# Performance work log

Hardware: AMD Instinct MI355X
Metric: run time of the kernel (lower is better)

The kernel has to match this reference:

```python
import jax, jax.numpy as jnp
import numpy as np

B, N, C, H = 4, 1024, 768, 12
D = C // H  # head_dim = 64
EPS_BN = 1e-5


def setup_inputs() -> dict:
    key = jax.random.key(0)
    ks = jax.random.split(key, 8)
    s = np.float32(D ** -0.5)
    return {
        "x": jax.random.normal(ks[0], (B, N, C), dtype=jnp.float32),
        "qkv_w": jax.random.normal(ks[1], (3 * C, C), dtype=jnp.float32) * (C ** -0.5),
        "qkv_b": jnp.zeros((3 * C,), dtype=jnp.float32),
        "proj_w": jax.random.normal(ks[2], (C, C), dtype=jnp.float32) * (C ** -0.5),
        "proj_b": jnp.zeros((C,), dtype=jnp.float32),
        "scale": jnp.asarray(s),
        "riem_scale": jnp.asarray(s),
        "grass_scale": jnp.asarray(s),
        "conv_w": jax.random.normal(ks[3], (H, 3 * H), dtype=jnp.float32) * ((3 * H) ** -0.5),
        "conv_b": jnp.zeros((H,), dtype=jnp.float32),
        "bn_gamma": jnp.ones((H,), dtype=jnp.float32),
        "bn_beta": jnp.zeros((H,), dtype=jnp.float32),
        "bn_mean": jnp.zeros((H,), dtype=jnp.float32),
        "bn_var": jnp.ones((H,), dtype=jnp.float32),
    }


def reference(x, qkv_w, qkv_b, proj_w, proj_b, scale, riem_scale, grass_scale,
              conv_w, conv_b, bn_gamma, bn_beta, bn_mean, bn_var):
    Bx, Nx, Cx = x.shape
    # qkv projection -> [3, B, H, N, D]
    qkv = (x @ qkv_w.T + qkv_b).reshape(Bx, Nx, 3, H, D).transpose(2, 0, 3, 1, 4)
    q, k, v = qkv[0], qkv[1], qkv[2]

    # Grassmannian points: reduced QR over each [N, D] token matrix
    qgr, _ = jnp.linalg.qr(q)
    kgr, _ = jnp.linalg.qr(k)
    # dots [B,H,N,N]; norm over singleton dim == abs, then squared -> dots**2
    dots = jnp.einsum('bhnd,bhmd->bhnm', qgr, kgr)
    attn_grass = (dots * dots) * grass_scale

    # standard scaled dot-product scores
    qk = jnp.einsum('bhnd,bhmd->bhnm', q, k)
    attn = qk * scale

    # covariance Frobenius distance between rank-1 covariances q_i q_i^T, k_j k_j^T:
    # ||q q^T - k k^T||_F^2 = |q|^4 + |k|^4 - 2 (q.k)^2 ; similarity = -sqrt(.)
    qn2 = jnp.sum(q * q, axis=-1)  # [B,H,N]
    kn2 = jnp.sum(k * k, axis=-1)  # [B,H,N]
    d2 = qn2[..., :, None] ** 2 + kn2[..., None, :] ** 2 - 2.0 * (qk * qk)
    attn_riem = -jnp.sqrt(jnp.maximum(d2, 0.0) + 1e-8) * riem_scale

    # concat over head-channel dim -> [B, 3H, N, N], 1x1 conv + BatchNorm (eval stats)
    cat = jnp.concatenate([attn, attn_riem, attn_grass], axis=1)
    y = jnp.einsum('bcnm,oc->bonm', cat, conv_w) + conv_b[None, :, None, None]
    inv = (bn_gamma / jnp.sqrt(bn_var + EPS_BN))[None, :, None, None]
    y = (y - bn_mean[None, :, None, None]) * inv + bn_beta[None, :, None, None]

    p = jax.nn.softmax(y, axis=-1)
    out = jnp.einsum('bhnm,bhmd->bhnd', p, v)  # [B,H,N,D]
    out = out.transpose(0, 2, 1, 3).reshape(Bx, Nx, Cx)
    return out @ proj_w.T + proj_b
```

## Files before the change

kernel.cpp:

```cpp
#include <hip/hip_runtime.h>
#include <math.h>


typedef __attribute__((ext_vector_type(8))) short short8;
typedef __attribute__((ext_vector_type(4))) float f32x4;

__device__ __forceinline__ unsigned bf16r(float x) {
    unsigned u = __float_as_uint(x);
    return (u + 0x7FFFu + ((u >> 16) & 1u)) >> 16;
}
__device__ __forceinline__ unsigned packhl(float x) {
    unsigned u = __float_as_uint(x);
    unsigned hi = (u + 0x7FFFu + ((u >> 16) & 1u)) & 0xFFFF0000u;
    float lo = x - __uint_as_float(hi);
    unsigned ul = __float_as_uint(lo);
    unsigned l16 = (ul + 0x7FFFu + ((ul >> 16) & 1u)) >> 16;
    return hi | (l16 & 0xFFFFu);
}
__device__ __forceinline__ uint4 pack4(float4 v) {
    uint4 o;
    o.x = packhl(v.x); o.y = packhl(v.y); o.z = packhl(v.z); o.w = packhl(v.w);
    return o;
}
__device__ __forceinline__ float unpackhl(unsigned u) {
    return __uint_as_float(u & 0xFFFF0000u) + __uint_as_float(u << 16);
}
union U4S8 { uint4 u; short8 s; };
__device__ __forceinline__ short8 mk_hi(uint4 a, uint4 b) {
    U4S8 r;
    r.u.x = __builtin_amdgcn_perm(a.y, a.x, 0x07060302);
    r.u.y = __builtin_amdgcn_perm(a.w, a.z, 0x07060302);
    r.u.z = __builtin_amdgcn_perm(b.y, b.x, 0x07060302);
    r.u.w = __builtin_amdgcn_perm(b.w, b.z, 0x07060302);
    return r.s;
}
__device__ __forceinline__ short8 mk_lo(uint4 a, uint4 b) {
    U4S8 r;
    r.u.x = __builtin_amdgcn_perm(a.y, a.x, 0x05040100);
    r.u.y = __builtin_amdgcn_perm(a.w, a.z, 0x05040100);
    r.u.z = __builtin_amdgcn_perm(b.y, b.x, 0x05040100);
    r.u.w = __builtin_amdgcn_perm(b.w, b.z, 0x05040100);
    return r.s;
}
__device__ __forceinline__ uint4 ld4v(const unsigned* vp, int mbase, int d) {
    uint4 r;
    r.x = vp[(size_t)(mbase + 0) * 64 + d];
    r.y = vp[(size_t)(mbase + 1) * 64 + d];
    r.z = vp[(size_t)(mbase + 2) * 64 + d];
    r.w = vp[(size_t)(mbase + 3) * 64 + d];
    return r;
}
#define MFMA(a,b,c) __builtin_amdgcn_mfma_f32_16x16x32_bf16(a, b, c, 0, 0, 0)

__global__ __launch_bounds__(256) void qkv_mfma(
    const float* __restrict__ x, const float* __restrict__ wsrc,
    const float* __restrict__ bias,
    float* __restrict__ q, float* __restrict__ k,
    unsigned* __restrict__ qpk, unsigned* __restrict__ kpk, unsigned* __restrict__ vpk)
{
    __shared__ unsigned xT[32 * 64];
    __shared__ unsigned wT[64 * 64];
    const int tid = threadIdx.x;
    const int lane = tid & 63;
    const int w = tid >> 6;
    const int rowL = lane & 15;
    const int g = lane >> 4;
    const int r7 = rowL & 7;
    const int n0 = blockIdx.x * 64;
    const int m0 = blockIdx.y * 32;
    f32x4 accA = {0,0,0,0}, accB = {0,0,0,0};

    for (int kk0 = 0; kk0 < 768; kk0 += 64) {
        __syncthreads();
#pragma unroll
        for (int e = 0; e < 2; e++) {
            int ci = tid + 256 * e; int R = ci >> 4, c = ci & 15;
            float4 fv = *(const float4*)&x[(size_t)(m0 + R) * 768 + kk0 + c * 4];
            *(uint4*)&xT[R * 64 + ((c ^ (R & 7)) << 2)] = pack4(fv);
        }
#pragma unroll
        for (int e = 0; e < 4; e++) {
            int ci = tid + 256 * e; int R = ci >> 4, c = ci & 15;
            float4 fv = *(const float4*)&wsrc[(size_t)(n0 + R) * 768 + kk0 + c * 4];
            *(uint4*)&wT[R * 64 + ((c ^ (R & 7)) << 2)] = pack4(fv);
        }
        __syncthreads();
#pragma unroll
        for (int ks = 0; ks < 2; ks++) {
            int c0 = ks * 8 + g * 2;
            uint4 b0 = *(const uint4*)&wT[(w * 16 + rowL) * 64 + ((c0 ^ r7) << 2)];
            uint4 b1 = *(const uint4*)&wT[(w * 16 + rowL) * 64 + (((c0 + 1) ^ r7) << 2)];
            short8 whi = mk_hi(b0, b1), wlo = mk_lo(b0, b1);
            uint4 a0 = *(const uint4*)&xT[rowL * 64 + ((c0 ^ r7) << 2)];
            uint4 a1 = *(const uint4*)&xT[rowL * 64 + (((c0 + 1) ^ r7) << 2)];
            short8 xhi = mk_hi(a0, a1), xlo = mk_lo(a0, a1);
            accA = MFMA(xhi, whi, accA);
            accA = MFMA(xhi, wlo, accA);
            accA = MFMA(xlo, whi, accA);
            uint4 a2 = *(const uint4*)&xT[(16 + rowL) * 64 + ((c0 ^ r7) << 2)];
            uint4 a3 = *(const uint4*)&xT[(16 + rowL) * 64 + (((c0 + 1) ^ r7) << 2)];
            short8 xhi2 = mk_hi(a2, a3), xlo2 = mk_lo(a2, a3);
            accB = MFMA(xhi2, whi, accB);
            accB = MFMA(xhi2, wlo, accB);
            accB = MFMA(xlo2, whi, accB);
        }
    }
    const int col = n0 + w * 16 + rowL;
    const float bv = bias[col];
    const int s = (n0 >= 1536) ? 2 : ((n0 >= 768) ? 1 : 0);
    const int hc = col - s * 768;
    const int head = hc >> 6;
    const int cin = hc & 63;
#pragma unroll
    for (int half = 0; half < 2; half++) {
        f32x4 acc = half ? accB : accA;
#pragma unroll
        for (int r = 0; r < 4; r++) {
            int row = m0 + half * 16 + g * 4 + r;
            int bb = row >> 10, n = row & 1023;
            size_t idx = ((size_t)(bb * 12 + head) << 16) + ((size_t)n << 6) + cin;
            float val = acc[r] + bv;
            if (s == 0)      { q[idx] = val; qpk[idx] = packhl(val); }
            else if (s == 1) { k[idx] = val; kpk[idx] = packhl(val); }
            else             { vpk[idx] = packhl(val); }
        }
    }
}

__global__ __launch_bounds__(256) void proj_mfma(
    const unsigned* __restrict__ apk, const float* __restrict__ wsrc,
    const float* __restrict__ bias, float* __restrict__ out)
{
    __shared__ unsigned xT[32 * 64];
    __shared__ unsigned wT[64 * 64];
    const int tid = threadIdx.x;
    const int lane = tid & 63;
    const int w = tid >> 6;
    const int rowL = lane & 15;
    const int g = lane >> 4;
    const int r7 = rowL & 7;
    const int n0 = blockIdx.x * 64;
    const int m0 = blockIdx.y * 32;
    f32x4 accA = {0,0,0,0}, accB = {0,0,0,0};

    for (int kk0 = 0; kk0 < 768; kk0 += 64) {
        __syncthreads();
#pragma unroll
        for (int e = 0; e < 2; e++) {
            int ci = tid + 256 * e; int R = ci >> 4, c = ci & 15;
            uint4 v = *(const uint4*)&apk[(size_t)(m0 + R) * 768 + kk0 + c * 4];
            *(uint4*)&xT[R * 64 + ((c ^ (R & 7)) << 2)] = v;
        }
#pragma unroll
        for (int e = 0; e < 4; e++) {
            int ci = tid + 256 * e; int R = ci >> 4, c = ci & 15;
            float4 fv = *(const float4*)&wsrc[(size_t)(n0 + R) * 768 + kk0 + c * 4];
            *(uint4*)&wT[R * 64 + ((c ^ (R & 7)) << 2)] = pack4(fv);
        }
        __syncthreads();
#pragma unroll
        for (int ks = 0; ks < 2; ks++) {
            int c0 = ks * 8 + g * 2;
            uint4 b0 = *(const uint4*)&wT[(w * 16 + rowL) * 64 + ((c0 ^ r7) << 2)];
            uint4 b1 = *(const uint4*)&wT[(w * 16 + rowL) * 64 + (((c0 + 1) ^ r7) << 2)];
            short8 whi = mk_hi(b0, b1), wlo = mk_lo(b0, b1);
            uint4 a0 = *(const uint4*)&xT[rowL * 64 + ((c0 ^ r7) << 2)];
            uint4 a1 = *(const uint4*)&xT[rowL * 64 + (((c0 + 1) ^ r7) << 2)];
            short8 xhi = mk_hi(a0, a1), xlo = mk_lo(a0, a1);
            accA = MFMA(xhi, whi, accA);
            accA = MFMA(xhi, wlo, accA);
            accA = MFMA(xlo, whi, accA);
            uint4 a2 = *(const uint4*)&xT[(16 + rowL) * 64 + ((c0 ^ r7) << 2)];
            uint4 a3 = *(const uint4*)&xT[(16 + rowL) * 64 + (((c0 + 1) ^ r7) << 2)];
            short8 xhi2 = mk_hi(a2, a3), xlo2 = mk_lo(a2, a3);
            accB = MFMA(xhi2, whi, accB);
            accB = MFMA(xhi2, wlo, accB);
            accB = MFMA(xlo2, whi, accB);
        }
    }
    const int col = n0 + w * 16 + rowL;
    const float bv = bias[col];
#pragma unroll
    for (int half = 0; half < 2; half++) {
        f32x4 acc = half ? accB : accA;
#pragma unroll
        for (int r = 0; r < 4; r++) {
            int row = m0 + half * 16 + g * 4 + r;
            out[(size_t)row * 768 + col] = acc[r] + bv;
        }
    }
}

__global__ __launch_bounds__(256) void row_norms(
    const float* __restrict__ q, const float* __restrict__ k,
    float* __restrict__ qn4, float* __restrict__ kn4)
{
    int wid = blockIdx.x * 4 + (threadIdx.x >> 6);
    int lane = threadIdx.x & 63;
    const float* src; float* dst; int r;
    if (wid < 49152) { src = q; dst = qn4; r = wid; }
    else             { src = k; dst = kn4; r = wid - 49152; }
    float xv = src[(size_t)r * 64 + lane];
    float s = xv * xv;
#pragma unroll
    for (int m = 1; m < 64; m <<= 1) s += __shfl_xor(s, m, 64);
    if (lane == 0) dst[r] = s * s;
}

__global__ __launch_bounds__(1024)
__attribute__((amdgpu_waves_per_eu(4, 4)))
void qr_fact(const float* __restrict__ q, const float* __restrict__ k,
             unsigned* __restrict__ Vp_, float* __restrict__ taug)
{
    const int id = blockIdx.x;
    const float* src = (id & 1) ? k : q;
    src += (size_t)(id >> 1) << 16;
    unsigned* Vp = Vp_ + (size_t)id * 65536;
    const int tid = threadIdx.x;
    const int lane = tid & 63;
    const int w = tid >> 6;
    __shared__ float vbufA[1024];
    __shared__ float vbufB[1024];
    __shared__ float taub[64];

    float a[4][16];
#pragma unroll
    for (int c = 0; c < 4; c++)
#pragma unroll
        for (int i = 0; i < 16; i++)
            a[c][i] = src[(i * 64 + lane) * 64 + 4 * w + c];

    if (w == 0) {
        float part = 0.f;
#pragma unroll
        for (int i = 0; i < 16; i++) part += a[0][i] * a[0][i];
#pragma unroll
        for (int m = 1; m < 64; m <<= 1) part += __shfl_xor(part, m, 64);
        float sigma = part;
        float xd = __shfl(a[0][0], 0, 64);
        float nrm = sqrtf(sigma);
        float beta = (xd >= 0.f) ? -nrm : nrm;
        float vd = xd - beta;
        float vtv = (sigma - xd * xd) + vd * vd;
        float tau2 = (vtv > 0.f) ? 2.f / vtv : 0.f;
        if (lane == 0) a[0][0] = vd;
#pragma unroll
        for (int i = 0; i < 16; i++) vbufA[i * 64 + lane] = a[0][i];
        if (lane == 0) taub[0] = tau2;
    }
    __syncthreads();

    for (int d = 0; d < 64; d++) {
        const int jb = 4 * w;
        if (jb + 3 > d) {
            float* vb = (d & 1) ? vbufB : vbufA;
            float vr[16];
#pragma unroll
            for (int i = 0; i < 16; i++) vr[i] = vb[i * 64 + lane];
            float t2 = taub[d];
            float dp0 = 0.f, dp1 = 0.f, dp2 = 0.f, dp3 = 0.f;
#pragma unroll
            for (int i = 0; i < 16; i++) {
                dp0 += vr[i] * a[0][i];
                dp1 += vr[i] * a[1][i];
                dp2 += vr[i] * a[2][i];
                dp3 += vr[i] * a[3][i];
            }
#pragma unroll
            for (int m = 1; m < 64; m <<= 1) {
                dp0 += __shfl_xor(dp0, m, 64);
                dp1 += __shfl_xor(dp1, m, 64);
                dp2 += __shfl_xor(dp2, m, 64);
                dp3 += __shfl_xor(dp3, m, 64);
            }
            float s0 = t2 * dp0, s1 = t2 * dp1, s2 = t2 * dp2, s3 = t2 * dp3;
            if (jb + 0 > d) {
#pragma unroll
                for (int i = 0; i < 16; i++) a[0][i] -= s0 * vr[i];
            }
            if (jb + 1 > d) {
#pragma unroll
                for (int i = 0; i < 16; i++) a[1][i] -= s1 * vr[i];
            }
            if (jb + 2 > d) {
#pragma unroll
                for (int i = 0; i < 16; i++) a[2][i] -= s2 * vr[i];
            }
            {
#pragma unroll
                for (int i = 0; i < 16; i++) a[3][i] -= s3 * vr[i];
            }
        }
        if (d < 63) {
            const int dn = d + 1;
            if (w == (dn >> 2)) {
                const int cd = dn & 3;
#pragma unroll
                for (int c = 0; c < 4; c++) if (c == cd) {
                    float part = 0.f;
#pragma unroll
                    for (int i = 0; i < 16; i++) {
                        int r = i * 64 + lane;
                        float xx = a[c][i];
                        part += (r >= dn) ? xx * xx : 0.f;
                    }
#pragma unroll
                    for (int m = 1; m < 64; m <<= 1) part += __shfl_xor(part, m, 64);
                    float sigma = part;
                    float xd = __shfl(a[c][0], dn, 64);
                    float nrm = sqrtf(sigma);
                    float beta = (xd >= 0.f) ? -nrm : nrm;
                    float vd = xd - beta;
                    float vtv = (sigma - xd * xd) + vd * vd;
                    float tau2 = (vtv > 0.f) ? 2.f / vtv : 0.f;
                    if (lane == dn) a[c][0] = vd;
                    float* vbn = (dn & 1) ? vbufB : vbufA;
#pragma unroll
                    for (int i = 0; i < 16; i++) {
                        int r = i * 64 + lane;
                        vbn[i * 64 + lane] = (r < dn) ? 0.f : a[c][i];
                    }
                    if (lane == 0) taub[dn] = tau2;
                }
            }
        }
        __syncthreads();
    }

    if (tid < 64) taug[id * 64 + tid] = taub[tid];
#pragma unroll
    for (int c = 0; c < 4; c++) {
        int j = 4 * w + c;
#pragma unroll
        for (int i = 0; i < 16; i++) {
            int r = i * 64 + lane;
            float vv = (r < j) ? 0.f : a[c][i];
            Vp[(size_t)j * 1024 + r] = packhl(vv);
        }
    }
}

__global__ __launch_bounds__(256) void qr_gpart(
    const unsigned* __restrict__ Vp_, float* __restrict__ Gpart)
{
    const int id = blockIdx.x;
    const int sl = blockIdx.y;
    const unsigned* Vp = Vp_ + (size_t)id * 65536;
    __shared__ unsigned Vc[64 * 32];
    const int tid = threadIdx.x;
    const int lane = tid & 63;
    const int w = tid >> 6;
    const int rowL = lane & 15;
    const int g = lane >> 4;

    f32x4 acc0 = {0,0,0,0}, acc1 = {0,0,0,0}, acc2 = {0,0,0,0}, acc3 = {0,0,0,0};
    for (int r0 = sl * 256; r0 < sl * 256 + 256; r0 += 32) {
        __syncthreads();
#pragma unroll
        for (int e = 0; e < 2; e++) {
            int ci = tid + 256 * e;
            int row = ci >> 3, c = ci & 7;
            uint4 v = *(const uint4*)&Vp[(size_t)row * 1024 + r0 + c * 4];
            *(uint4*)&Vc[row * 32 + ((c ^ (row & 7)) << 2)] = v;
        }
        __syncthreads();
        int ra = w * 16 + rowL;
        uint4 a0 = *(const uint4*)&Vc[ra * 32 + (((g * 2) ^ (ra & 7)) << 2)];
        uint4 a1 = *(const uint4*)&Vc[ra * 32 + (((g * 2 + 1) ^ (ra & 7)) << 2)];
        short8 Ahi = mk_hi(a0, a1), Alo = mk_lo(a0, a1);
#define GDO(jt, accv) { int rb = jt * 16 + rowL; \
        uint4 b0 = *(const uint4*)&Vc[rb * 32 + (((g * 2) ^ (rb & 7)) << 2)]; \
        uint4 b1 = *(const uint4*)&Vc[rb * 32 + (((g * 2 + 1) ^ (rb & 7)) << 2)]; \
        short8 Bhi = mk_hi(b0, b1), Blo = mk_lo(b0, b1); \
        accv = MFMA(Ahi, Bhi, accv); accv = MFMA(Ahi, Blo, accv); accv = MFMA(Alo, Bhi, accv); }
        GDO(0, acc0) GDO(1, acc1) GDO(2, acc2) GDO(3, acc3)
#undef GDO
    }
    float* dst = Gpart + ((size_t)(id * 4 + sl) << 12);
#define GWR(jt, accv) { \
    dst[(w * 16 + g * 4 + 0) * 64 + jt * 16 + rowL] = accv[0]; \
    dst[(w * 16 + g * 4 + 1) * 64 + jt * 16 + rowL] = accv[1]; \
    dst[(w * 16 + g * 4 + 2) * 64 + jt * 16 + rowL] = accv[2]; \
    dst[(w * 16 + g * 4 + 3) * 64 + jt * 16 + rowL] = accv[3]; }
    GWR(0, acc0) GWR(1, acc1) GWR(2, acc2) GWR(3, acc3)
#undef GWR
}

__global__ __launch_bounds__(256) void qr_tw2(
    const unsigned* __restrict__ Vp_, const float* __restrict__ taug,
    const float* __restrict__ Gpart, float* __restrict__ Wg)
{
    const int id = blockIdx.x;
    const unsigned* Vp = Vp_ + (size_t)id * 65536;
    __shared__ float G_s[64 * 65];
    __shared__ float wbuf[64];
    __shared__ float tau_s[64];
    const int tid = threadIdx.x;
    if (tid < 64) tau_s[tid] = taug[id * 64 + tid];
    const float* Gp = Gpart + ((size_t)(id * 4) << 12);
#pragma unroll
    for (int e = 0; e < 16; e++) {
        int idx = tid + 256 * e;
        float sum = Gp[idx] + Gp[4096 + idx] + Gp[8192 + idx] + Gp[12288 + idx];
        G_s[(idx >> 6) * 65 + (idx & 63)] = sum;
    }
    const int i = tid >> 2;
    const int cq = tid & 3;
    float regA[16];
#pragma unroll
    for (int cc = 0; cc < 16; cc++)
        regA[cc] = unpackhl(Vp[(size_t)i * 1024 + cq * 16 + cc]);
    __syncthreads();
    for (int j = 63; j >= 0; j--) {
        if (i == j) {
            float tj = tau_s[j];
#pragma unroll
            for (int cc = 0; cc < 16; cc++) {
                regA[cc] *= tj;
                wbuf[cq * 16 + cc] = regA[cc];
            }
        }
        __syncthreads();
        if (i < j) {
            float gij = G_s[i * 65 + j];
#pragma unroll
            for (int cc = 0; cc < 16; cc++)
                regA[cc] = fmaf(-gij, wbuf[cq * 16 + cc], regA[cc]);
        }
        __syncthreads();
    }
#pragma unroll
    for (int cc = 0; cc < 16; cc++)
        Wg[(size_t)id * 4096 + i * 64 + cq * 16 + cc] = regA[cc];
}

__global__ __launch_bounds__(256) void qr_formq(
    const unsigned* __restrict__ Vp_, const float* __restrict__ Wg,
    unsigned short* __restrict__ qgrh, unsigned short* __restrict__ kgrh)
{
    const int id = blockIdx.x;
    const int rb = blockIdx.y;
    const unsigned* Vp = Vp_ + (size_t)id * 65536;
    const float* Wm = Wg + (size_t)id * 4096;
    unsigned short* dst = ((id & 1) ? kgrh : qgrh) + ((size_t)(id >> 1) << 16);
    __shared__ float Vl[64 * 65];
    __shared__ float Wl[64 * 64];
    const int tid = threadIdx.x;
    const int rbase = rb * 64;
#pragma unroll
    for (int e = 0; e < 16; e++) {
        int idx = tid + 256 * e;
        int j = idx >> 6, rl = idx & 63;
        Vl[rl * 65 + j] = unpackhl(Vp[(size_t)j * 1024 + rbase + rl]);
        Wl[idx] = Wm[idx];
    }
    __syncthreads();
    const int rl = tid >> 2;
    const int cg = (tid & 3) << 4;
    const int rglob = rbase + rl;
    unsigned short outv[16];
#pragma unroll
    for (int cc = 0; cc < 16; cc++) {
        int c = cg + cc;
        float s = (rglob == c) ? 1.f : 0.f;
        for (int j = 0; j < 64; j++) s -= Vl[rl * 65 + j] * Wl[j * 64 + c];
        outv[cc] = (unsigned short)bf16r(s);
    }
#pragma unroll
    for (int cc = 0; cc < 16; cc += 4)
        *(ushort4*)&dst[(size_t)rglob * 64 + cg + cc] = *(ushort4*)&outv[cc];
}

#define SC_EACH12(F) F(0) F(1) F(2) F(3) F(4) F(5) F(6) F(7) F(8) F(9) F(10) F(11)
#define SC_DECLY(o) float y##o##_0 = 0.f, y##o##_1 = 0.f, y##o##_2 = 0.f, y##o##_3 = 0.f;
#define SC_LOADC(o) const float cA##o = cw[o * 36 + h], \
                                cB##o = cw[o * 36 + 12 + h], \
                                cC##o = cw[o * 36 + 24 + h];
#define SC_CONV1(o,r) y##o##_##r = fmaf(cA##o, att, fmaf(cB##o, rie, fmaf(cC##o, gra, y##o##_##r)));
#define SC_CONVROW(r) SC_CONV1(0,r) SC_CONV1(1,r) SC_CONV1(2,r) SC_CONV1(3,r) SC_CONV1(4,r) SC_CONV1(5,r) \
                      SC_CONV1(6,r) SC_CONV1(7,r) SC_CONV1(8,r) SC_CONV1(9,r) SC_CONV1(10,r) SC_CONV1(11,r)
#define SC_SCORE(r) { \
    float qk = s1[r], gr = s2[r]; \
    float qn4v = qn4s[g * 4 + r]; \
    float att = qk * scale; \
    float d2 = qn4v + kn4v - 2.f * qk * qk; \
    float rie = -sqrtf(fmaxf(d2, 0.f) + 1e-8f) * riem_scale; \
    float gra = gr * gr * grass_scale; \
    SC_CONVROW(r) }
#define SC_OUT(o) { \
    float inv = bn_gamma[o] * rsqrtf(bn_var[o] + 1e-5f); \
    float Bb = fmaf(conv_b[o] - bn_mean[o], inv, bn_beta[o]); \
    float* dst = Sbuf + ((size_t)(z * 12 + o) * 1024 + n0) * 1024 + m0 + w * 16 + rowL; \
    dst[(size_t)(g * 4 + 0) * 1024] = fmaf(y##o##_0, inv, Bb); \
    dst[(size_t)(g * 4 + 1) * 1024] = fmaf(y##o##_1, inv, Bb); \
    dst[(size_t)(g * 4 + 2) * 1024] = fmaf(y##o##_2, inv, Bb); \
    dst[(size_t)(g * 4 + 3) * 1024] = fmaf(y##o##_3, inv, Bb); }

__global__ __launch_bounds__(256) void sattn_scores(
    const unsigned* __restrict__ qpk, const unsigned* __restrict__ kpk,
    const unsigned short* __restrict__ qgrh, const unsigned short* __restrict__ kgrh,
    const float* __restrict__ qn4g, const float* __restrict__ kn4g,
    const float* __restrict__ cw, const float* __restrict__ conv_b,
    const float* __restrict__ bn_gamma, const float* __restrict__ bn_beta,
    const float* __restrict__ bn_mean, const float* __restrict__ bn_var,
    const float* __restrict__ scale_p, const float* __restrict__ riem_p,
    const float* __restrict__ grass_p, float* __restrict__ Sbuf, int b0)
{
    __shared__ unsigned qT[16 * 64];
    __shared__ unsigned short qgT[16 * 64];
    __shared__ unsigned kL[64 * 64];
    __shared__ unsigned short kgrL[64 * 64];
    __shared__ float qn4s[16];
    __shared__ float kn4s[64];

    const int tid = threadIdx.x;
    const int lane = tid & 63;
    const int w = tid >> 6;
    const int rowL = lane & 15;
    const int g = lane >> 4;
    const int r7 = rowL & 7;
    const int m0 = blockIdx.x * 64;
    const int n0 = blockIdx.y * 16;
    const int z = blockIdx.z;
    const int b = b0 + z;
    const float scale = scale_p[0], riem_scale = riem_p[0], grass_scale = grass_p[0];

    SC_EACH12(SC_DECLY)

    for (int h = 0; h < 12; h++) {
        __syncthreads();
        {
            int R = tid >> 4, c = tid & 15;
            uint4 v = *(const uint4*)&qpk[((size_t)(b * 12 + h) << 16) + (size_t)(n0 + R) * 64 + c * 4];
            *(uint4*)&qT[R * 64 + ((c ^ (R & 7)) << 2)] = v;
        }
        if (tid < 128) {
            int R = tid >> 3, c = tid & 7;
            uint4 v = *(const uint4*)&qgrh[((size_t)(b * 12 + h) << 16) + (size_t)(n0 + R) * 64 + c * 8];
            *(uint4*)&qgT[R * 64 + ((c ^ (R & 7)) << 3)] = v;
        }
#pragma unroll
        for (int e = 0; e < 4; e++) {
            int ci = tid + 256 * e; int m = ci >> 4, c = ci & 15;
            uint4 v = *(const uint4*)&kpk[((size_t)(b * 12 + h) << 16) + (size_t)(m0 + m) * 64 + c * 4];
            *(uint4*)&kL[m * 64 + ((c ^ (m & 7)) << 2)] = v;
        }
#pragma unroll
        for (int e = 0; e < 2; e++) {
            int ci = tid + 256 * e; int m = ci >> 3, c = ci & 7;
            uint4 v = *(const uint4*)&kgrh[((size_t)(b * 12 + h) << 16) + (size_t)(m0 + m) * 64 + c * 8];
            *(uint4*)&kgrL[m * 64 + ((c ^ (m & 7)) << 3)] = v;
        }
        if (tid < 64) kn4s[tid] = kn4g[(size_t)(b * 12 + h) * 1024 + m0 + tid];
        if (tid < 16) qn4s[tid] = qn4g[(size_t)(b * 12 + h) * 1024 + n0 + tid];
        __syncthreads();

        float kn4v = kn4s[w * 16 + rowL];
        f32x4 s1 = {0,0,0,0}, s2 = {0,0,0,0};
#pragma unroll
        for (int ks = 0; ks < 2; ks++) {
            int c0 = ks * 8 + g * 2;
            uint4 a0 = *(const uint4*)&qT[rowL * 64 + ((c0 ^ r7) << 2)];
            uint4 a1 = *(const uint4*)&qT[rowL * 64 + (((c0 + 1) ^ r7) << 2)];
            uint4 b0v = *(const uint4*)&kL[(w * 16 + rowL) * 64 + ((c0 ^ r7) << 2)];
            uint4 b1v = *(const uint4*)&kL[(w * 16 + rowL) * 64 + (((c0 + 1) ^ r7) << 2)];
            short8 qhi = mk_hi(a0, a1), qlo = mk_lo(a0, a1);
            short8 khi = mk_hi(b0v, b1v), klo = mk_lo(b0v, b1v);
            s1 = MFMA(qhi, khi, s1);
            s1 = MFMA(qhi, klo, s1);
            s1 = MFMA(qlo, khi, s1);
            int cg = ks * 4 + g;
            short8 qg = *(const short8*)&qgT[rowL * 64 + ((cg ^ r7) << 3)];
            short8 kg2 = *(const short8*)&kgrL[(w * 16 + rowL) * 64 + ((cg ^ r7) << 3)];
            s2 = MFMA(qg, kg2, s2);
        }
        SC_EACH12(SC_LOADC)
        SC_SCORE(0) SC_SCORE(1) SC_SCORE(2) SC_SCORE(3)
    }
    SC_EACH12(SC_OUT)
}

__global__ __launch_bounds__(256) void sattn_pv(
    const unsigned* __restrict__ vpk, const float* __restrict__ Sbuf,
    unsigned* __restrict__ attno_pk, int b0)
{
    __shared__ unsigned short P_s[16 * 64];
    __shared__ unsigned vt_s[64 * 64];
    __shared__ float mrun[16], lrun[16], cos_[16];

    const int tid = threadIdx.x;
    const int lane = tid & 63;
    const int w = tid >> 6;
    const int rowL = lane & 15;
    const int g = lane >> 4;
    const int r7 = rowL & 7;
    const int n0 = blockIdx.x * 16;
    const int o = blockIdx.y;
    const int z = blockIdx.z;
    const int b = b0 + z;
    const int srow = tid >> 4;
    const int sc4 = (tid & 15) * 4;

    if (tid < 16) { mrun[tid] = -1e30f; lrun[tid] = 0.f; }
    f32x4 acc = {0,0,0,0};
    const float* Srow = Sbuf + ((size_t)(z * 12 + o) * 1024 + n0 + srow) * 1024;
    const unsigned* vp = vpk + ((size_t)(b * 12 + o) << 16);
    __syncthreads();

    for (int m0 = 0; m0 < 1024; m0 += 64) {
        float4 sv = *(const float4*)&Srow[m0 + sc4];
        float mx = fmaxf(fmaxf(sv.x, sv.y), fmaxf(sv.z, sv.w));
        mx = fmaxf(mx, __shfl_xor(mx, 1, 64));
        mx = fmaxf(mx, __shfl_xor(mx, 2, 64));
        mx = fmaxf(mx, __shfl_xor(mx, 4, 64));
        mx = fmaxf(mx, __shfl_xor(mx, 8, 64));
        float mo = mrun[srow];
        float mn = fmaxf(mo, mx);
        float co = expf(mo - mn);
        float p0 = expf(sv.x - mn), p1 = expf(sv.y - mn), p2 = expf(sv.z - mn), p3 = expf(sv.w - mn);
        unsigned u0 = bf16r(p0), u1 = bf16r(p1), u2 = bf16r(p2), u3 = bf16r(p3);
        {
            ushort4 pw = make_ushort4((unsigned short)u0, (unsigned short)u1,
                                      (unsigned short)u2, (unsigned short)u3);
            *(ushort4*)&P_s[srow * 64 + (((sc4 >> 3) ^ (srow & 7)) << 3) + (sc4 & 7)] = pw;
        }
        float ps = __uint_as_float(u0 << 16) + __uint_as_float(u1 << 16)
                 + __uint_as_float(u2 << 16) + __uint_as_float(u3 << 16);
        ps += __shfl_xor(ps, 1, 64); ps += __shfl_xor(ps, 2, 64);
        ps += __shfl_xor(ps, 4, 64); ps += __shfl_xor(ps, 8, 64);
        if ((lane & 15) == 0) {
            mrun[srow] = mn;
            cos_[srow] = co;
            lrun[srow] = lrun[srow] * co + ps;
        }
#pragma unroll
        for (int e = 0; e < 4; e++) {
            int d_ = tid & 63;
            int mb = (tid >> 6) * 4 + 16 * e;
            int mc = (tid >> 6) + 4 * e;
            uint4 v = ld4v(vp + (size_t)m0 * 64, mb, d_);
            *(uint4*)&vt_s[d_ * 64 + ((mc ^ (d_ & 15)) << 2)] = v;
        }
        __syncthreads();
        {
            float c0_ = cos_[g * 4 + 0], c1_ = cos_[g * 4 + 1];
            float c2_ = cos_[g * 4 + 2], c3_ = cos_[g * 4 + 3];
            acc[0] *= c0_; acc[1] *= c1_; acc[2] *= c2_; acc[3] *= c3_;
        }
        const int d_ = w * 16 + rowL;
        const unsigned* vrow = &vt_s[d_ * 64];
#pragma unroll
        for (int kk = 0; kk < 2; kk++) {
            int mc8 = kk * 4 + g;
            short8 pa = *(const short8*)&P_s[rowL * 64 + ((mc8 ^ r7) << 3)];
            int c0 = kk * 8 + g * 2;
            uint4 b0v = *(const uint4*)&vrow[((c0 ^ (d_ & 15)) << 2)];
            uint4 b1v = *(const uint4*)&vrow[(((c0 + 1) ^ (d_ & 15)) << 2)];
            short8 vh = mk_hi(b0v, b1v), vl = mk_lo(b0v, b1v);
            acc = MFMA(pa, vh, acc);
            acc = MFMA(pa, vl, acc);
        }
        __syncthreads();
    }
#pragma unroll
    for (int r = 0; r < 4; r++) {
        int row = g * 4 + r;
        size_t idx = ((size_t)(b * 1024 + n0 + row)) * 768 + o * 64 + w * 16 + rowL;
        attno_pk[idx] = packhl(acc[r] / lrun[row]);
    }
}

extern "C" void kernel_launch(void* const* d_in, const int* in_sizes, int n_in,
                              void* d_out, int out_size, void* d_ws, size_t ws_size,
                              hipStream_t stream) {
    const float* x          = (const float*)d_in[0];
    const float* qkv_w      = (const float*)d_in[1];
    const float* qkv_b      = (const float*)d_in[2];
    const float* proj_w     = (const float*)d_in[3];
    const float* proj_b     = (const float*)d_in[4];
    const float* scale      = (const float*)d_in[5];
    const float* riem_scale = (const float*)d_in[6];
    const float* grass_scale= (const float*)d_in[7];
    const float* conv_w     = (const float*)d_in[8];
    const float* conv_b     = (const float*)d_in[9];
    const float* bn_gamma   = (const float*)d_in[10];
    const float* bn_beta    = (const float*)d_in[11];
    const float* bn_mean    = (const float*)d_in[12];
    const float* bn_var     = (const float*)d_in[13];
    float* out = (float*)d_out;

    float* q   = (float*)d_ws;
    float* k   = q + 3145728;
    unsigned* qpk = (unsigned*)(k + 3145728);
    unsigned* kpk = qpk + 3145728;
    unsigned* vpk = kpk + 3145728;
    unsigned short* qgrh = (unsigned short*)(vpk + 3145728);
    unsigned short* kgrh = qgrh + 3145728;
    float* qn4 = (float*)(kgrh + 3145728);
    float* kn4 = qn4 + 49152;
    unsigned* attno_pk = (unsigned*)q;

    const size_t BASE = 75890688ull;
    const size_t SB1  = 50331648ull;
    float* Sbuf = (float*)((char*)d_ws + BASE);
    unsigned* Vpk2 = (unsigned*)((char*)d_ws + BASE);
    float* Wg   = (float*)(Vpk2 + 96 * 65536);
    float* taug = Wg + 96 * 4096;
    float* Gpart = taug + 96 * 64;
    const bool full = (ws_size >= BASE + 4 * SB1);

    hipLaunchKernelGGL(qkv_mfma, dim3(36, 128), dim3(256), 0, stream,
                       x, qkv_w, qkv_b, q, k, qpk, kpk, vpk);
    hipLaunchKernelGGL(row_norms, dim3(24576), dim3(256), 0, stream, q, k, qn4, kn4);

    hipLaunchKernelGGL(qr_fact, dim3(96), dim3(1024), 0, stream, q, k, Vpk2, taug);
    hipLaunchKernelGGL(qr_gpart, dim3(96, 4), dim3(256), 0, stream, Vpk2, Gpart);
    hipLaunchKernelGGL(qr_tw2, dim3(96), dim3(256), 0, stream, Vpk2, taug, Gpart, Wg);
    hipLaunchKernelGGL(qr_formq, dim3(96, 16), dim3(256), 0, stream, Vpk2, Wg, qgrh, kgrh);

    if (full) {
        hipLaunchKernelGGL(sattn_scores, dim3(16, 64, 4), dim3(256), 0, stream,
                           qpk, kpk, qgrh, kgrh, qn4, kn4, conv_w, conv_b,
                           bn_gamma, bn_beta, bn_mean, bn_var,
                           scale, riem_scale, grass_scale, Sbuf, 0);
        hipLaunchKernelGGL(sattn_pv, dim3(64, 12, 4), dim3(256), 0, stream,
                           vpk, Sbuf, attno_pk, 0);
    } else {
        for (int b = 0; b < 4; b++) {
            hipLaunchKernelGGL(sattn_scores, dim3(16, 64, 1), dim3(256), 0, stream,
                               qpk, kpk, qgrh, kgrh, qn4, kn4, conv_w, conv_b,
                               bn_gamma, bn_beta, bn_mean, bn_var,
                               scale, riem_scale, grass_scale, Sbuf, b);
            hipLaunchKernelGGL(sattn_pv, dim3(64, 12, 1), dim3(256), 0, stream,
                               vpk, Sbuf, attno_pk, b);
        }
    }

    hipLaunchKernelGGL(proj_mfma, dim3(12, 128), dim3(256), 0, stream,
                       attno_pk, proj_w, proj_b, out);
}
```

Before: 683.2 us.

## Pre-pack GEMM operands to hi/lo bf16 once and enlarge qkv tile

Adds a pack_f32 kernel that converts x, qkv_w and proj_w into packed hi/lo bf16 words once, so the qkv and projection GEMMs load pre-packed tiles instead of repeating the split per block. The qkv GEMM tile grows from 32 to 64 rows, with four accumulators per wave, to reuse each weight tile across more rows. This adds extra kernel launches and a round trip through workspace memory, and raises register and LDS use in the qkv kernel.

```diff
diff --git a/kernel.cpp b/kernel.cpp
--- a/kernel.cpp
+++ b/kernel.cpp
@@ -16,11 +16,6 @@
     unsigned ul = __float_as_uint(lo);
     unsigned l16 = (ul + 0x7FFFu + ((ul >> 16) & 1u)) >> 16;
     return hi | (l16 & 0xFFFFu);
-}
-__device__ __forceinline__ uint4 pack4(float4 v) {
-    uint4 o;
-    o.x = packhl(v.x); o.y = packhl(v.y); o.z = packhl(v.z); o.w = packhl(v.w);
-    return o;
 }
 __device__ __forceinline__ float unpackhl(unsigned u) {
     return __uint_as_float(u & 0xFFFF0000u) + __uint_as_float(u << 16);
@@ -52,11 +47,92 @@
 }
 #define MFMA(a,b,c) __builtin_amdgcn_mfma_f32_16x16x32_bf16(a, b, c, 0, 0, 0)
 
+__global__ __launch_bounds__(256) void pack_f32(
+    const float* __restrict__ src, unsigned* __restrict__ dst, int n4)
+{
+    int i = blockIdx.x * 256 + threadIdx.x;
+    if (i < n4) {
+        float4 v = *(const float4*)&src[(size_t)i * 4];
+        uint4 o;
+        o.x = packhl(v.x); o.y = packhl(v.y); o.z = packhl(v.z); o.w = packhl(v.w);
+        *(uint4*)&dst[(size_t)i * 4] = o;
+    }
+}
+
 __global__ __launch_bounds__(256) void qkv_mfma(
-    const float* __restrict__ x, const float* __restrict__ wsrc,
+    const unsigned* __restrict__ xpk, const unsigned* __restrict__ wpk,
     const float* __restrict__ bias,
     float* __restrict__ q, float* __restrict__ k,
     unsigned* __restrict__ qpk, unsigned* __restrict__ kpk, unsigned* __restrict__ vpk)
+{
+    __shared__ unsigned xT[64 * 64];
+    __shared__ unsigned wT[64 * 64];
+    const int tid = threadIdx.x;
+    const int lane = tid & 63;
+    const int w = tid >> 6;
+    const int rowL = lane & 15;
+    const int g = lane >> 4;
+    const int r7 = rowL & 7;
+    const int n0 = blockIdx.x * 64;
+    const int m0 = blockIdx.y * 64;
+    f32x4 acc0 = {0,0,0,0}, acc1 = {0,0,0,0}, acc2 = {0,0,0,0}, acc3 = {0,0,0,0};
+
+    for (int kk0 = 0; kk0 < 768; kk0 += 64) {
+        __syncthreads();
+#pragma unroll
+        for (int e = 0; e < 4; e++) {
+            int ci = tid + 256 * e; int R = ci >> 4, c = ci & 15;
+            uint4 v = *(const uint4*)&xpk[(size_t)(m0 + R) * 768 + kk0 + c * 4];
+            *(uint4*)&xT[R * 64 + ((c ^ (R & 7)) << 2)] = v;
+        }
+#pragma unroll
+        for (int e = 0; e < 4; e++) {
+            int ci = tid + 256 * e; int R = ci >> 4, c = ci & 15;
+            uint4 v = *(const uint4*)&wpk[(size_t)(n0 + R) * 768 + kk0 + c * 4];
+            *(uint4*)&wT[R * 64 + ((c ^ (R & 7)) << 2)] = v;
+        }
+        __syncthreads();
+#pragma unroll
+        for (int ks = 0; ks < 2; ks++) {
+            int c0 = ks * 8 + g * 2;
+            uint4 b0 = *(const uint4*)&wT[(w * 16 + rowL) * 64 + ((c0 ^ r7) << 2)];
+            uint4 b1 = *(const uint4*)&wT[(w * 16 + rowL) * 64 + (((c0 + 1) ^ r7) << 2)];
+            short8 whi = mk_hi(b0, b1), wlo = mk_lo(b0, b1);
+#define QFRAG(f, accv) { \
+            uint4 a0 = *(const uint4*)&xT[(f * 16 + rowL) * 64 + ((c0 ^ r7) << 2)]; \
+            uint4 a1 = *(const uint4*)&xT[(f * 16 + rowL) * 64 + (((c0 + 1) ^ r7) << 2)]; \
+            short8 xhi = mk_hi(a0, a1), xlo = mk_lo(a0, a1); \
+            accv = MFMA(xhi, whi, accv); \
+            accv = MFMA(xhi, wlo, accv); \
+            accv = MFMA(xlo, whi, accv); }
+            QFRAG(0, acc0) QFRAG(1, acc1) QFRAG(2, acc2) QFRAG(3, acc3)
+#undef QFRAG
+        }
+    }
+    const int col = n0 + w * 16 + rowL;
+    const float bv = bias[col];
+    const int s = (n0 >= 1536) ? 2 : ((n0 >= 768) ? 1 : 0);
+    const int hc = col - s * 768;
+    const int head = hc >> 6;
+    const int cin = hc & 63;
+#define QOUT(f, accv) { \
+    _Pragma("unroll") \
+    for (int r = 0; r < 4; r++) { \
+        int row = m0 + f * 16 + g * 4 + r; \
+        int bb = row >> 10, n = row & 1023; \
+        size_t idx = ((size_t)(bb * 12 + head) << 16) + ((size_t)n << 6) + cin; \
+        float val = accv[r] + bv; \
+        if (s == 0)      { q[idx] = val; qpk[idx] = packhl(val); } \
+        else if (s == 1) { k[idx] = val; kpk[idx] = packhl(val); } \
+        else             { vpk[idx] = packhl(val); } \
+    } }
+    QOUT(0, acc0) QOUT(1, acc1) QOUT(2, acc2) QOUT(3, acc3)
+#undef QOUT
+}
+
+__global__ __launch_bounds__(256) void proj_mfma(
+    const unsigned* __restrict__ apk, const unsigned* __restrict__ wpk,
+    const float* __restrict__ bias, float* __restrict__ out)
 {
     __shared__ unsigned xT[32 * 64];
     __shared__ unsigned wT[64 * 64];
@@ -75,87 +151,14 @@
 #pragma unroll
         for (int e = 0; e < 2; e++) {
             int ci = tid + 256 * e; int R = ci >> 4, c = ci & 15;
-            float4 fv = *(const float4*)&x[(size_t)(m0 + R) * 768 + kk0 + c * 4];
-            *(uint4*)&xT[R * 64 + ((c ^ (R & 7)) << 2)] = pack4(fv);
+            uint4 v = *(const uint4*)&apk[(size_t)(m0 + R) * 768 + kk0 + c * 4];
+            *(uint4*)&xT[R * 64 + ((c ^ (R & 7)) << 2)] = v;
         }
 #pragma unroll
         for (int e = 0; e < 4; e++) {
             int ci = tid + 256 * e; int R = ci >> 4, c = ci & 15;
-            float4 fv = *(const float4*)&wsrc[(size_t)(n0 + R) * 768 + kk0 + c * 4];
-            *(uint4*)&wT[R * 64 + ((c ^ (R & 7)) << 2)] = pack4(fv);
-        }
-        __syncthreads();
-#pragma unroll
-        for (int ks = 0; ks < 2; ks++) {
-            int c0 = ks * 8 + g * 2;
-            uint4 b0 = *(const uint4*)&wT[(w * 16 + rowL) * 64 + ((c0 ^ r7) << 2)];
-            uint4 b1 = *(const uint4*)&wT[(w * 16 + rowL) * 64 + (((c0 + 1) ^ r7) << 2)];
-            short8 whi = mk_hi(b0, b1), wlo = mk_lo(b0, b1);
-            uint4 a0 = *(const uint4*)&xT[rowL * 64 + ((c0 ^ r7) << 2)];
-            uint4 a1 = *(const uint4*)&xT[rowL * 64 + (((c0 + 1) ^ r7) << 2)];
-            short8 xhi = mk_hi(a0, a1), xlo = mk_lo(a0, a1);
-            accA = MFMA(xhi, whi, accA);
-            accA = MFMA(xhi, wlo, accA);
-            accA = MFMA(xlo, whi, accA);
-            uint4 a2 = *(const uint4*)&xT[(16 + rowL) * 64 + ((c0 ^ r7) << 2)];
-            uint4 a3 = *(const uint4*)&xT[(16 + rowL) * 64 + (((c0 + 1) ^ r7) << 2)];
-            short8 xhi2 = mk_hi(a2, a3), xlo2 = mk_lo(a2, a3);
-            accB = MFMA(xhi2, whi, accB);
-            accB = MFMA(xhi2, wlo, accB);
-            accB = MFMA(xlo2, whi, accB);
-        }
-    }
-    const int col = n0 + w * 16 + rowL;
-    const float bv = bias[col];
-    const int s = (n0 >= 1536) ? 2 : ((n0 >= 768) ? 1 : 0);
-    const int hc = col - s * 768;
-    const int head = hc >> 6;
-    const int cin = hc & 63;
-#pragma unroll
-    for (int half = 0; half < 2; half++) {
-        f32x4 acc = half ? accB : accA;
-#pragma unroll
-        for (int r = 0; r < 4; r++) {
-            int row = m0 + half * 16 + g * 4 + r;
-            int bb = row >> 10, n = row & 1023;
-            size_t idx = ((size_t)(bb * 12 + head) << 16) + ((size_t)n << 6) + cin;
-            float val = acc[r] + bv;
-            if (s == 0)      { q[idx] = val; qpk[idx] = packhl(val); }
-            else if (s == 1) { k[idx] = val; kpk[idx] = packhl(val); }
-            else             { vpk[idx] = packhl(val); }
-        }
-    }
-}
-
-__global__ __launch_bounds__(256) void proj_mfma(
-    const unsigned* __restrict__ apk, const float* __restrict__ wsrc,
-    const float* __restrict__ bias, float* __restrict__ out)
-{
-    __shared__ unsigned xT[32 * 64];
-    __shared__ unsigned wT[64 * 64];
-    const int tid = threadIdx.x;
-    const int lane = tid & 63;
-    const int w = tid >> 6;
-    const int rowL = lane & 15;
-    const int g = lane >> 4;
-    const int r7 = rowL & 7;
-    const int n0 = blockIdx.x * 64;
-    const int m0 = blockIdx.y * 32;
-    f32x4 accA = {0,0,0,0}, accB = {0,0,0,0};
-
-    for (int kk0 = 0; kk0 < 768; kk0 += 64) {
-        __syncthreads();
-#pragma unroll
-        for (int e = 0; e < 2; e++) {
-            int ci = tid + 256 * e; int R = ci >> 4, c = ci & 15;
-            uint4 v = *(const uint4*)&apk[(size_t)(m0 + R) * 768 + kk0 + c * 4];
-            *(uint4*)&xT[R * 64 + ((c ^ (R & 7)) << 2)] = v;
-        }
-#pragma unroll
-        for (int e = 0; e < 4; e++) {
-            int ci = tid + 256 * e; int R = ci >> 4, c = ci & 15;
-            float4 fv = *(const float4*)&wsrc[(size_t)(n0 + R) * 768 + kk0 + c * 4];
-            *(uint4*)&wT[R * 64 + ((c ^ (R & 7)) << 2)] = pack4(fv);
+            uint4 v = *(const uint4*)&wpk[(size_t)(n0 + R) * 768 + kk0 + c * 4];
+            *(uint4*)&wT[R * 64 + ((c ^ (R & 7)) << 2)] = v;
         }
         __syncthreads();
 #pragma unroll
@@ -699,24 +702,31 @@
     float* qn4 = (float*)(kgrh + 3145728);
     float* kn4 = qn4 + 49152;
     unsigned* attno_pk = (unsigned*)q;
+    unsigned* ppk = (unsigned*)k;
 
     const size_t BASE = 75890688ull;
     const size_t SB1  = 50331648ull;
     float* Sbuf = (float*)((char*)d_ws + BASE);
+    unsigned* xpk_ = (unsigned*)((char*)d_ws + BASE);
+    unsigned* wpk_ = xpk_ + 3145728;
     unsigned* Vpk2 = (unsigned*)((char*)d_ws + BASE);
     float* Wg   = (float*)(Vpk2 + 96 * 65536);
     float* taug = Wg + 96 * 4096;
     float* Gpart = taug + 96 * 64;
     const bool full = (ws_size >= BASE + 4 * SB1);
 
-    hipLaunchKernelGGL(qkv_mfma, dim3(36, 128), dim3(256), 0, stream,
-                       x, qkv_w, qkv_b, q, k, qpk, kpk, vpk);
+    hipLaunchKernelGGL(pack_f32, dim3(3072), dim3(256), 0, stream, x, xpk_, 786432);
+    hipLaunchKernelGGL(pack_f32, dim3(1728), dim3(256), 0, stream, qkv_w, wpk_, 442368);
+    hipLaunchKernelGGL(qkv_mfma, dim3(36, 64), dim3(256), 0, stream,
+                       xpk_, wpk_, qkv_b, q, k, qpk, kpk, vpk);
     hipLaunchKernelGGL(row_norms, dim3(24576), dim3(256), 0, stream, q, k, qn4, kn4);
 
     hipLaunchKernelGGL(qr_fact, dim3(96), dim3(1024), 0, stream, q, k, Vpk2, taug);
     hipLaunchKernelGGL(qr_gpart, dim3(96, 4), dim3(256), 0, stream, Vpk2, Gpart);
     hipLaunchKernelGGL(qr_tw2, dim3(96), dim3(256), 0, stream, Vpk2, taug, Gpart, Wg);
     hipLaunchKernelGGL(qr_formq, dim3(96, 16), dim3(256), 0, stream, Vpk2, Wg, qgrh, kgrh);
+
+    hipLaunchKernelGGL(pack_f32, dim3(576), dim3(256), 0, stream, proj_w, ppk, 147456);
 
     if (full) {
         hipLaunchKernelGGL(sattn_scores, dim3(16, 64, 4), dim3(256), 0, stream,
@@ -737,5 +747,5 @@
     }
 
     hipLaunchKernelGGL(proj_mfma, dim3(12, 128), dim3(256), 0, stream,
-                       attno_pk, proj_w, proj_b, out);
-}
+                       attno_pk, ppk, proj_b, out);
+}
```

Result: no change. 693.4 us (+1.5%).

## Pre-pack GEMM operands to bf16 pairs and enlarge score tile to 32 rows

Applied to the files above, without the earlier changes.

Adds a pack_f32 kernel that converts x, qkv_w and proj_w once into hi/lo bf16 packed words, so the qkv and proj GEMMs no longer repeat the split conversion in every tile load. The sattn_scores kernel now uses 512 threads and 32 query rows per block, so each loaded K tile is reused across twice as many rows and the grid is halved. The trade-off is three extra launches plus the memory traffic of the packed copies, and higher shared memory and register pressure per block in the scores kernel. The packed buffers reuse workspace regions (the Sbuf area and the k buffer) and rely on those regions not being live at the time.

```diff
diff --git a/kernel.cpp b/kernel.cpp
--- a/kernel.cpp
+++ b/kernel.cpp
@@ -16,11 +16,6 @@
     unsigned ul = __float_as_uint(lo);
     unsigned l16 = (ul + 0x7FFFu + ((ul >> 16) & 1u)) >> 16;
     return hi | (l16 & 0xFFFFu);
-}
-__device__ __forceinline__ uint4 pack4(float4 v) {
-    uint4 o;
-    o.x = packhl(v.x); o.y = packhl(v.y); o.z = packhl(v.z); o.w = packhl(v.w);
-    return o;
 }
 __device__ __forceinline__ float unpackhl(unsigned u) {
     return __uint_as_float(u & 0xFFFF0000u) + __uint_as_float(u << 16);
@@ -52,8 +47,20 @@
 }
 #define MFMA(a,b,c) __builtin_amdgcn_mfma_f32_16x16x32_bf16(a, b, c, 0, 0, 0)
 
+__global__ __launch_bounds__(256) void pack_f32(
+    const float* __restrict__ src, unsigned* __restrict__ dst, int n4)
+{
+    int i = blockIdx.x * 256 + threadIdx.x;
+    if (i < n4) {
+        float4 v = *(const float4*)&src[(size_t)i * 4];
+        uint4 o;
+        o.x = packhl(v.x); o.y = packhl(v.y); o.z = packhl(v.z); o.w = packhl(v.w);
+        *(uint4*)&dst[(size_t)i * 4] = o;
+    }
+}
+
 __global__ __launch_bounds__(256) void qkv_mfma(
-    const float* __restrict__ x, const float* __restrict__ wsrc,
+    const unsigned* __restrict__ xpk, const unsigned* __restrict__ wpk,
     const float* __restrict__ bias,
     float* __restrict__ q, float* __restrict__ k,
     unsigned* __restrict__ qpk, unsigned* __restrict__ kpk, unsigned* __restrict__ vpk)
@@ -75,14 +82,14 @@
 #pragma unroll
         for (int e = 0; e < 2; e++) {
             int ci = tid + 256 * e; int R = ci >> 4, c = ci & 15;
-            float4 fv = *(const float4*)&x[(size_t)(m0 + R) * 768 + kk0 + c * 4];
-            *(uint4*)&xT[R * 64 + ((c ^ (R & 7)) << 2)] = pack4(fv);
+            uint4 v = *(const uint4*)&xpk[(size_t)(m0 + R) * 768 + kk0 + c * 4];
+            *(uint4*)&xT[R * 64 + ((c ^ (R & 7)) << 2)] = v;
         }
 #pragma unroll
         for (int e = 0; e < 4; e++) {
             int ci = tid + 256 * e; int R = ci >> 4, c = ci & 15;
-            float4 fv = *(const float4*)&wsrc[(size_t)(n0 + R) * 768 + kk0 + c * 4];
-            *(uint4*)&wT[R * 64 + ((c ^ (R & 7)) << 2)] = pack4(fv);
+            uint4 v = *(const uint4*)&wpk[(size_t)(n0 + R) * 768 + kk0 + c * 4];
+            *(uint4*)&wT[R * 64 + ((c ^ (R & 7)) << 2)] = v;
         }
         __syncthreads();
 #pragma unroll
@@ -128,7 +135,7 @@
 }
 
 __global__ __launch_bounds__(256) void proj_mfma(
-    const unsigned* __restrict__ apk, const float* __restrict__ wsrc,
+    const unsigned* __restrict__ apk, const unsigned* __restrict__ wpk,
     const float* __restrict__ bias, float* __restrict__ out)
 {
     __shared__ unsigned xT[32 * 64];
@@ -154,8 +161,8 @@
 #pragma unroll
         for (int e = 0; e < 4; e++) {
             int ci = tid + 256 * e; int R = ci >> 4, c = ci & 15;
-            float4 fv = *(const float4*)&wsrc[(size_t)(n0 + R) * 768 + kk0 + c * 4];
-            *(uint4*)&wT[R * 64 + ((c ^ (R & 7)) << 2)] = pack4(fv);
+            uint4 v = *(const uint4*)&wpk[(size_t)(n0 + R) * 768 + kk0 + c * 4];
+            *(uint4*)&wT[R * 64 + ((c ^ (R & 7)) << 2)] = v;
         }
         __syncthreads();
 #pragma unroll
@@ -481,7 +488,7 @@
                       SC_CONV1(6,r) SC_CONV1(7,r) SC_CONV1(8,r) SC_CONV1(9,r) SC_CONV1(10,r) SC_CONV1(11,r)
 #define SC_SCORE(r) { \
     float qk = s1[r], gr = s2[r]; \
-    float qn4v = qn4s[g * 4 + r]; \
+    float qn4v = qn4s[ng * 16 + g * 4 + r]; \
     float att = qk * scale; \
     float d2 = qn4v + kn4v - 2.f * qk * qk; \
     float rie = -sqrtf(fmaxf(d2, 0.f) + 1e-8f) * riem_scale; \
@@ -490,13 +497,13 @@
 #define SC_OUT(o) { \
     float inv = bn_gamma[o] * rsqrtf(bn_var[o] + 1e-5f); \
     float Bb = fmaf(conv_b[o] - bn_mean[o], inv, bn_beta[o]); \
-    float* dst = Sbuf + ((size_t)(z * 12 + o) * 1024 + n0) * 1024 + m0 + w * 16 + rowL; \
+    float* dst = Sbuf + ((size_t)(z * 12 + o) * 1024 + n0 + ng * 16) * 1024 + m0 + mq * 16 + rowL; \
     dst[(size_t)(g * 4 + 0) * 1024] = fmaf(y##o##_0, inv, Bb); \
     dst[(size_t)(g * 4 + 1) * 1024] = fmaf(y##o##_1, inv, Bb); \
     dst[(size_t)(g * 4 + 2) * 1024] = fmaf(y##o##_2, inv, Bb); \
     dst[(size_t)(g * 4 + 3) * 1024] = fmaf(y##o##_3, inv, Bb); }
 
-__global__ __launch_bounds__(256) void sattn_scores(
+__global__ __launch_bounds__(512) void sattn_scores(
     const unsigned* __restrict__ qpk, const unsigned* __restrict__ kpk,
     const unsigned short* __restrict__ qgrh, const unsigned short* __restrict__ kgrh,
     const float* __restrict__ qn4g, const float* __restrict__ kn4g,
@@ -506,21 +513,23 @@
     const float* __restrict__ scale_p, const float* __restrict__ riem_p,
     const float* __restrict__ grass_p, float* __restrict__ Sbuf, int b0)
 {
-    __shared__ unsigned qT[16 * 64];
-    __shared__ unsigned short qgT[16 * 64];
+    __shared__ unsigned qT[32 * 64];
+    __shared__ unsigned short qgT[32 * 64];
     __shared__ unsigned kL[64 * 64];
     __shared__ unsigned short kgrL[64 * 64];
-    __shared__ float qn4s[16];
+    __shared__ float qn4s[32];
     __shared__ float kn4s[64];
 
     const int tid = threadIdx.x;
     const int lane = tid & 63;
-    const int w = tid >> 6;
+    const int w8 = tid >> 6;
+    const int mq = w8 & 3;
+    const int ng = w8 >> 2;
     const int rowL = lane & 15;
     const int g = lane >> 4;
     const int r7 = rowL & 7;
     const int m0 = blockIdx.x * 64;
-    const int n0 = blockIdx.y * 16;
+    const int n0 = blockIdx.y * 32;
     const int z = blockIdx.z;
     const int b = b0 + z;
     const float scale = scale_p[0], riem_scale = riem_p[0], grass_scale = grass_p[0];
@@ -534,44 +543,43 @@
             uint4 v = *(const uint4*)&qpk[((size_t)(b * 12 + h) << 16) + (size_t)(n0 + R) * 64 + c * 4];
             *(uint4*)&qT[R * 64 + ((c ^ (R & 7)) << 2)] = v;
         }
-        if (tid < 128) {
+        if (tid < 256) {
             int R = tid >> 3, c = tid & 7;
             uint4 v = *(const uint4*)&qgrh[((size_t)(b * 12 + h) << 16) + (size_t)(n0 + R) * 64 + c * 8];
             *(uint4*)&qgT[R * 64 + ((c ^ (R & 7)) << 3)] = v;
         }
 #pragma unroll
-        for (int e = 0; e < 4; e++) {
-            int ci = tid + 256 * e; int m = ci >> 4, c = ci & 15;
+        for (int e = 0; e < 2; e++) {
+            int ci = tid + 512 * e; int m = ci >> 4, c = ci & 15;
             uint4 v = *(const uint4*)&kpk[((size_t)(b * 12 + h) << 16) + (size_t)(m0 + m) * 64 + c * 4];
             *(uint4*)&kL[m * 64 + ((c ^ (m & 7)) << 2)] = v;
         }
-#pragma unroll
-        for (int e = 0; e < 2; e++) {
-            int ci = tid + 256 * e; int m = ci >> 3, c = ci & 7;
+        {
+            int ci = tid; int m = ci >> 3, c = ci & 7;
             uint4 v = *(const uint4*)&kgrh[((size_t)(b * 12 + h) << 16) + (size_t)(m0 + m) * 64 + c * 8];
             *(uint4*)&kgrL[m * 64 + ((c ^ (m & 7)) << 3)] = v;
         }
         if (tid < 64) kn4s[tid] = kn4g[(size_t)(b * 12 + h) * 1024 + m0 + tid];
-        if (tid < 16) qn4s[tid] = qn4g[(size_t)(b * 12 + h) * 1024 + n0 + tid];
-        __syncthreads();
-
-        float kn4v = kn4s[w * 16 + rowL];
+        if (tid < 32) qn4s[tid] = qn4g[(size_t)(b * 12 + h) * 1024 + n0 + tid];
+        __syncthreads();
+
+        float kn4v = kn4s[mq * 16 + rowL];
         f32x4 s1 = {0,0,0,0}, s2 = {0,0,0,0};
 #pragma unroll
         for (int ks = 0; ks < 2; ks++) {
             int c0 = ks * 8 + g * 2;
-            uint4 a0 = *(const uint4*)&qT[rowL * 64 + ((c0 ^ r7) << 2)];
-            uint4 a1 = *(const uint4*)&qT[rowL * 64 + (((c0 + 1) ^ r7) << 2)];
-            uint4 b0v = *(const uint4*)&kL[(w * 16 + rowL) * 64 + ((c0 ^ r7) << 2)];
-            uint4 b1v = *(const uint4*)&kL[(w * 16 + rowL) * 64 + (((c0 + 1) ^ r7) << 2)];
+            uint4 a0 = *(const uint4*)&qT[(ng * 16 + rowL) * 64 + ((c0 ^ r7) << 2)];
+            uint4 a1 = *(const uint4*)&qT[(ng * 16 + rowL) * 64 + (((c0 + 1) ^ r7) << 2)];
+            uint4 b0v = *(const uint4*)&kL[(mq * 16 + rowL) * 64 + ((c0 ^ r7) << 2)];
+            uint4 b1v = *(const uint4*)&kL[(mq * 16 + rowL) * 64 + (((c0 + 1) ^ r7) << 2)];
             short8 qhi = mk_hi(a0, a1), qlo = mk_lo(a0, a1);
             short8 khi = mk_hi(b0v, b1v), klo = mk_lo(b0v, b1v);
             s1 = MFMA(qhi, khi, s1);
             s1 = MFMA(qhi, klo, s1);
             s1 = MFMA(qlo, khi, s1);
-            int cg = ks * 4 + g;
-            short8 qg = *(const short8*)&qgT[rowL * 64 + ((cg ^ r7) << 3)];
-            short8 kg2 = *(const short8*)&kgrL[(w * 16 + rowL) * 64 + ((cg ^ r7) << 3)];
+            int cg2 = ks * 4 + g;
+            short8 qg = *(const short8*)&qgT[(ng * 16 + rowL) * 64 + ((cg2 ^ r7) << 3)];
+            short8 kg2 = *(const short8*)&kgrL[(mq * 16 + rowL) * 64 + ((cg2 ^ r7) << 3)];
             s2 = MFMA(qg, kg2, s2);
         }
         SC_EACH12(SC_LOADC)
@@ -699,18 +707,23 @@
     float* qn4 = (float*)(kgrh + 3145728);
     float* kn4 = qn4 + 49152;
     unsigned* attno_pk = (unsigned*)q;
+    unsigned* ppk = (unsigned*)k;
 
     const size_t BASE = 75890688ull;
     const size_t SB1  = 50331648ull;
     float* Sbuf = (float*)((char*)d_ws + BASE);
+    unsigned* xpk_ = (unsigned*)((char*)d_ws + BASE);
+    unsigned* wpk_ = xpk_ + 3145728;
     unsigned* Vpk2 = (unsigned*)((char*)d_ws + BASE);
     float* Wg   = (float*)(Vpk2 + 96 * 65536);
     float* taug = Wg + 96 * 4096;
     float* Gpart = taug + 96 * 64;
     const bool full = (ws_size >= BASE + 4 * SB1);
 
+    hipLaunchKernelGGL(pack_f32, dim3(3072), dim3(256), 0, stream, x, xpk_, 786432);
+    hipLaunchKernelGGL(pack_f32, dim3(1728), dim3(256), 0, stream, qkv_w, wpk_, 442368);
     hipLaunchKernelGGL(qkv_mfma, dim3(36, 128), dim3(256), 0, stream,
-                       x, qkv_w, qkv_b, q, k, qpk, kpk, vpk);
+                       xpk_, wpk_, qkv_b, q, k, qpk, kpk, vpk);
     hipLaunchKernelGGL(row_norms, dim3(24576), dim3(256), 0, stream, q, k, qn4, kn4);
 
     hipLaunchKernelGGL(qr_fact, dim3(96), dim3(1024), 0, stream, q, k, Vpk2, taug);
@@ -718,8 +731,10 @@
     hipLaunchKernelGGL(qr_tw2, dim3(96), dim3(256), 0, stream, Vpk2, taug, Gpart, Wg);
     hipLaunchKernelGGL(qr_formq, dim3(96, 16), dim3(256), 0, stream, Vpk2, Wg, qgrh, kgrh);
 
+    hipLaunchKernelGGL(pack_f32, dim3(576), dim3(256), 0, stream, proj_w, ppk, 147456);
+
     if (full) {
-        hipLaunchKernelGGL(sattn_scores, dim3(16, 64, 4), dim3(256), 0, stream,
+        hipLaunchKernelGGL(sattn_scores, dim3(16, 32, 4), dim3(512), 0, stream,
                            qpk, kpk, qgrh, kgrh, qn4, kn4, conv_w, conv_b,
                            bn_gamma, bn_beta, bn_mean, bn_var,
                            scale, riem_scale, grass_scale, Sbuf, 0);
@@ -727,7 +742,7 @@
                            vpk, Sbuf, attno_pk, 0);
     } else {
         for (int b = 0; b < 4; b++) {
-            hipLaunchKernelGGL(sattn_scores, dim3(16, 64, 1), dim3(256), 0, stream,
+            hipLaunchKernelGGL(sattn_scores, dim3(16, 32, 1), dim3(512), 0, stream,
                                qpk, kpk, qgrh, kgrh, qn4, kn4, conv_w, conv_b,
                                bn_gamma, bn_beta, bn_mean, bn_var,
                                scale, riem_scale, grass_scale, Sbuf, b);
@@ -737,5 +752,5 @@
     }
 
     hipLaunchKernelGGL(proj_mfma, dim3(12, 128), dim3(256), 0, stream,
-                       attno_pk, proj_w, proj_b, out);
-}
+                       attno_pk, ppk, proj_b, out);
+}
```

Result: faster. 596.1 us (median of 2 runs) (-12.7%).
